# Kernel optimization log

Measured on AMD Instinct MI355X. Metric: run time of the kernel, lower is better.

## Reference

```python
import jax, jax.numpy as jnp
import numpy as np

N_ROI = 116; G = 128; DEG = 32
N = G * N_ROI          # 14848 nodes
E = G * N_ROI * DEG    # 475136 edges
HID = 64; HEADS = 4; HC = HEADS * HID  # 256
EDIM = 5; EMB = 16; NG = 8; OUT = 2
NEG = 0.01      # nn.LeakyReLU default slope
NEG_ATT = 0.2   # GATv2 internal negative_slope
EPS = 1e-5


def leaky(x, s=NEG):
    return jnp.where(x >= 0, x, s * x)


def seg_softmax(logits, seg, n):
    # numerically stable softmax over edges grouped by target node
    m = jax.ops.segment_max(logits, seg, num_segments=n)
    m = jnp.where(jnp.isfinite(m), m, 0.0)
    ex = jnp.exp(logits - m[seg])
    s = jax.ops.segment_sum(ex, seg, num_segments=n)
    return ex / (s[seg] + 1e-16)


def _xav(k, shape):
    return jax.random.normal(k, shape, jnp.float32) * np.sqrt(2.0 / sum(shape)).astype(np.float32)


def setup_inputs() -> dict:
    key = jax.random.key(0)
    ks = jax.random.split(key, 40)
    x = jax.random.normal(ks[0], (N, N_ROI), jnp.float32)
    off = (jnp.arange(G, dtype=jnp.int32) * N_ROI)[:, None]
    src = (jax.random.randint(ks[1], (G, N_ROI * DEG), 0, N_ROI, jnp.int32) + off).reshape(-1)
    dst = (jax.random.randint(ks[2], (G, N_ROI * DEG), 0, N_ROI, jnp.int32) + off).reshape(-1)
    edge_index = jnp.stack([src, dst])  # [2, E], block-diagonal per graph
    edge_attr = jax.random.normal(ks[3], (E, EDIM), jnp.float32)
    grp = np.repeat(np.arange(NG, dtype=np.int32), [15] * 7 + [11])  # partition of 116 ROIs
    node_group = jnp.tile(jnp.asarray(grp), G)
    batch = jnp.repeat(jnp.arange(G, dtype=jnp.int32), N_ROI)
    p = {
        'group_emb': _xav(ks[4], (NG, EMB)),
        'W_embed': _xav(ks[5], (N_ROI + EMB, HID)), 'b_embed': jnp.zeros((HID,), jnp.float32),
        'We_enc': _xav(ks[6], (EDIM, HID)), 'be_enc': jnp.zeros((HID,), jnp.float32),
        'W1': _xav(ks[7], (HID, HID)), 'b1': jnp.zeros((HID,), jnp.float32),
        'W2': _xav(ks[8], (HID, HID)), 'b2': jnp.zeros((HID,), jnp.float32),
        'ln_g': jnp.ones((HID,), jnp.float32), 'ln_b': jnp.zeros((HID,), jnp.float32),
        'l0_Wl': _xav(ks[9], (HID, HC)), 'l0_Wr': _xav(ks[10], (HID, HC)),
        'l0_We': _xav(ks[11], (EDIM, HC)), 'l0_att': _xav(ks[12], (HEADS, HID)),
        'l0_b': jnp.zeros((HC,), jnp.float32),
        'l0_bn_g': jnp.ones((HC,), jnp.float32), 'l0_bn_b': jnp.zeros((HC,), jnp.float32),
        'l1_Wl': _xav(ks[13], (HC, HC)), 'l1_Wr': _xav(ks[14], (HC, HC)),
        'l1_We': _xav(ks[15], (EDIM, HC)), 'l1_att': _xav(ks[16], (HEADS, HID)),
        'l1_b': jnp.zeros((HC,), jnp.float32),
        'l1_bn_g': jnp.ones((HC,), jnp.float32), 'l1_bn_b': jnp.zeros((HC,), jnp.float32),
        'fc2_W': _xav(ks[17], (HC, OUT)), 'fc2_b': jnp.zeros((OUT,), jnp.float32),
    }
    return dict(x=x, edge_index=edge_index, edge_attr=edge_attr, batch=batch, node_group=node_group, **p)


def _gat_layer(h, src, dst, edge_attr, Wl, Wr, We, att, b, bn_g, bn_b):
    n = h.shape[0]
    xl = (h @ Wl).reshape(n, HEADS, HID)
    xr = (h @ Wr).reshape(n, HEADS, HID)
    e = (edge_attr @ We).reshape(-1, HEADS, HID)
    xls = xl[src]                                   # [E,H,C]
    z = leaky(xls + xr[dst] + e, NEG_ATT)
    logits = jnp.einsum('ehc,hc->eh', z, att)       # GATv2 attention scores
    alpha = seg_softmax(logits, dst, n)             # softmax over incoming edges per node
    out = jax.ops.segment_sum(xls * alpha[:, :, None], dst, num_segments=n)
    out = out.reshape(n, HC) + b
    mu = out.mean(0); var = ((out - mu) ** 2).mean(0)  # BatchNorm (batch stats)
    out = (out - mu) / jnp.sqrt(var + EPS) * bn_g + bn_b
    return leaky(out)


def reference(x, edge_index, edge_attr, batch, node_group, group_emb, W_embed, b_embed,
              We_enc, be_enc, W1, b1, W2, b2, ln_g, ln_b,
              l0_Wl, l0_Wr, l0_We, l0_att, l0_b, l0_bn_g, l0_bn_b,
              l1_Wl, l1_Wr, l1_We, l1_att, l1_b, l1_bn_g, l1_bn_b, fc2_W, fc2_b):
    src, dst = edge_index[0], edge_index[1]
    # BrainEncodeEmbed: group embedding concat + projection
    h = jnp.concatenate([x, group_emb[node_group]], axis=-1)   # [N, 132]
    h = leaky(h @ W_embed + b_embed)                            # [N, HID]
    eemb = leaky(edge_attr @ We_enc + be_enc)                   # [E, HID]
    # GINEConv: sum_j ReLU(x_j + e_ij), eps=0, then MLP
    msg = jax.nn.relu(h[src] + eemb)
    h = h + jax.ops.segment_sum(msg, dst, num_segments=N)
    h = leaky(h @ W1 + b1) @ W2 + b2
    h = leaky(h)
    mu = h.mean(-1, keepdims=True)
    v = ((h - mu) ** 2).mean(-1, keepdims=True)
    h = (h - mu) / jnp.sqrt(v + EPS) * ln_g + ln_b              # LayerNorm
    # stacked GATv2 blocks
    h = _gat_layer(h, src, dst, edge_attr, l0_Wl, l0_Wr, l0_We, l0_att, l0_b, l0_bn_g, l0_bn_b)
    h = _gat_layer(h, src, dst, edge_attr, l1_Wl, l1_Wr, l1_We, l1_att, l1_b, l1_bn_g, l1_bn_b)
    # global mean pool + classifier
    cnt = jax.ops.segment_sum(jnp.ones((h.shape[0],), h.dtype), batch, num_segments=G)
    pooled = jax.ops.segment_sum(h, batch, num_segments=G) / cnt[:, None]
    return pooled @ fc2_W + fc2_b
```

## Files before the change

### kernel.cpp

```cpp
#include <hip/hip_runtime.h>
#include <hip/hip_bf16.h>

#define NN     14848
#define NE     475136
#define NROI   116
#define NGRAPH 128
#define EPG    3712
#define HID    64
#define HC     256
#define NEG    0.01f
#define NEGA   0.2f
#define EPB    2304
#define XPADB  66

typedef __attribute__((ext_vector_type(8))) short short8;
typedef __attribute__((ext_vector_type(4))) float floatx4;
typedef __attribute__((ext_vector_type(2))) float floatx2;

__device__ __forceinline__ float leaky(float x, float s) { return fmaxf(x, s * x); }

__device__ __forceinline__ short f2bf(float f) {
    unsigned u = __float_as_uint(f);
    unsigned r = (u + 0x7fffu + ((u >> 16) & 1u)) >> 16;
    return (short)r;
}
__device__ __forceinline__ float bf2f(unsigned short b) {
    return __uint_as_float((unsigned)b << 16);
}

__global__ __launch_bounds__(256) void k_front(
    const float* __restrict__ x, const int* __restrict__ ng,
    const float* __restrict__ gemb, const float* __restrict__ W,
    const float* __restrict__ b, short* __restrict__ h0,
    const int* __restrict__ src, const int* __restrict__ dst,
    const float* __restrict__ ea,
    int* __restrict__ row_start, int* __restrict__ row_cnt,
    int* __restrict__ ssd, float* __restrict__ ea_s,
    float* __restrict__ stats01,
    const float* __restrict__ Wl0, const float* __restrict__ Wr0,
    const float* __restrict__ Wl1, const float* __restrict__ Wr1,
    short* __restrict__ Wt0, short* __restrict__ Wt1)
{
    const int tid = threadIdx.x;
    if (blockIdx.x < NGRAPH) {
        const int g = blockIdx.x;
        if (g < 2) {
            for (int i = tid; i < 512; i += 256) stats01[g * 512 + i] = 0.f;
        }
        const int e0 = g * EPG, nb = g * NROI;
        __shared__ int cnt[NROI], start[NROI], scn[128];
        __shared__ unsigned short pos[EPG];
        if (tid < NROI) cnt[tid] = 0;
        __syncthreads();
        for (int i = tid; i < EPG; i += 256) {
            const int dl = dst[e0 + i] - nb;
            pos[i] = (unsigned short)atomicAdd(&cnt[dl], 1);
        }
        __syncthreads();
        if (tid < 128) scn[tid] = (tid < NROI) ? cnt[tid] : 0;
        __syncthreads();
        #pragma unroll
        for (int off = 1; off < 128; off <<= 1) {
            int v = 0;
            if (tid < 128 && tid >= off) v = scn[tid - off];
            __syncthreads();
            if (tid < 128) scn[tid] += v;
            __syncthreads();
        }
        if (tid < NROI) {
            const int st = scn[tid] - cnt[tid];
            start[tid] = st;
            row_start[nb + tid] = e0 + st;
            row_cnt[nb + tid] = cnt[tid];
        }
        __syncthreads();
        for (int i = tid; i < EPG; i += 256) {
            const int e = e0 + i;
            const int dl = dst[e] - nb;
            const int gi = e0 + start[dl] + (int)pos[i];
            ssd[gi] = (src[e] - nb) | (dl << 16);
            const float4 q = make_float4(ea[e * 5], ea[e * 5 + 1], ea[e * 5 + 2], ea[e * 5 + 3]);
            *(float4*)&ea_s[(size_t)gi * 8] = q;
            ea_s[(size_t)gi * 8 + 4] = ea[e * 5 + 4];
        }
    } else if (blockIdx.x < NGRAPH + NN / 4) {
        const int w = tid >> 6, c = tid & 63;
        const int n = (blockIdx.x - NGRAPH) * 4 + w;
        __shared__ float in[4][132];
        for (int k = c; k < NROI; k += 64) in[w][k] = x[n * NROI + k];
        if (c < 16) in[w][NROI + c] = gemb[ng[n] * 16 + c];
        __syncthreads();
        float acc = b[c];
        #pragma unroll 4
        for (int k = 0; k < 132; k++) acc = fmaf(in[w][k], W[k * 64 + c], acc);
        h0[n * 64 + c] = f2bf(leaky(acc, NEG));
    } else {
        const int bb = blockIdx.x - (NGRAPH + NN / 4);
        if (bb < 512) {
            const int n = bb;
            for (int k = tid; k < 64; k += 256) {
                const float v = (n < 256) ? Wl0[k * 256 + n] : Wr0[k * 256 + (n - 256)];
                Wt0[(size_t)n * 64 + k] = f2bf(v);
            }
        } else {
            const int n = bb - 512;
            for (int k = tid; k < 256; k += 256) {
                const float v = (n < 256) ? Wl1[k * 256 + n] : Wr1[k * 256 + (n - 256)];
                Wt1[(size_t)n * 256 + k] = f2bf(v);
            }
        }
    }
}

__global__ __launch_bounds__(256) void k_gine_mlp_ln(
    const short* __restrict__ h0, const int* __restrict__ row_start,
    const int* __restrict__ row_cnt, const int* __restrict__ ssd,
    const float* __restrict__ ea_s,
    const float* __restrict__ We, const float* __restrict__ be,
    const float* __restrict__ W1, const float* __restrict__ b1,
    const float* __restrict__ W2, const float* __restrict__ b2,
    const float* __restrict__ lg_, const float* __restrict__ lb_,
    short* __restrict__ hn)
{
    const int tid = threadIdx.x, w = tid >> 6, lane = tid & 63;
    const int row = blockIdx.x * 4 + w;
    const int nb = (row / NROI) * NROI;
    const int st = row_start[row], cnt = row_cnt[row];
    const float w0 = We[lane], w1 = We[64 + lane], w2 = We[128 + lane],
                w3 = We[192 + lane], w4 = We[256 + lane];
    const float bec = be[lane];
    float g0 = 0.f, g1 = 0.f, g2 = 0.f, g3 = 0.f;
    int j = 0;
    for (; j + 4 <= cnt; j += 4) {
        const int i0 = st + j, i1 = st + j + 1, i2 = st + j + 2, i3 = st + j + 3;
        const int s0 = nb + (ssd[i0] & 0xffff), s1 = nb + (ssd[i1] & 0xffff),
                  s2 = nb + (ssd[i2] & 0xffff), s3 = nb + (ssd[i3] & 0xffff);
        const float h_0 = bf2f((unsigned short)h0[s0 * 64 + lane]),
                    h_1 = bf2f((unsigned short)h0[s1 * 64 + lane]),
                    h_2 = bf2f((unsigned short)h0[s2 * 64 + lane]),
                    h_3 = bf2f((unsigned short)h0[s3 * 64 + lane]);
        const float4 qa = *(const float4*)&ea_s[(size_t)i0 * 8];
        const float qa4 = ea_s[(size_t)i0 * 8 + 4];
        const float4 qb = *(const float4*)&ea_s[(size_t)i1 * 8];
        const float qb4 = ea_s[(size_t)i1 * 8 + 4];
        const float4 qc = *(const float4*)&ea_s[(size_t)i2 * 8];
        const float qc4 = ea_s[(size_t)i2 * 8 + 4];
        const float4 qd = *(const float4*)&ea_s[(size_t)i3 * 8];
        const float qd4 = ea_s[(size_t)i3 * 8 + 4];
        float e0_ = bec, e1_ = bec, e2_ = bec, e3_ = bec;
        e0_ = fmaf(qa.x, w0, e0_); e1_ = fmaf(qb.x, w0, e1_);
        e2_ = fmaf(qc.x, w0, e2_); e3_ = fmaf(qd.x, w0, e3_);
        e0_ = fmaf(qa.y, w1, e0_); e1_ = fmaf(qb.y, w1, e1_);
        e2_ = fmaf(qc.y, w1, e2_); e3_ = fmaf(qd.y, w1, e3_);
        e0_ = fmaf(qa.z, w2, e0_); e1_ = fmaf(qb.z, w2, e1_);
        e2_ = fmaf(qc.z, w2, e2_); e3_ = fmaf(qd.z, w2, e3_);
        e0_ = fmaf(qa.w, w3, e0_); e1_ = fmaf(qb.w, w3, e1_);
        e2_ = fmaf(qc.w, w3, e2_); e3_ = fmaf(qd.w, w3, e3_);
        e0_ = fmaf(qa4, w4, e0_);  e1_ = fmaf(qb4, w4, e1_);
        e2_ = fmaf(qc4, w4, e2_);  e3_ = fmaf(qd4, w4, e3_);
        g0 += fmaxf(h_0 + leaky(e0_, NEG), 0.f);
        g1 += fmaxf(h_1 + leaky(e1_, NEG), 0.f);
        g2 += fmaxf(h_2 + leaky(e2_, NEG), 0.f);
        g3 += fmaxf(h_3 + leaky(e3_, NEG), 0.f);
    }
    for (; j < cnt; j++) {
        const int idx = st + j;
        const int s = nb + (ssd[idx] & 0xffff);
        const float4 q = *(const float4*)&ea_s[(size_t)idx * 8];
        const float q4 = ea_s[(size_t)idx * 8 + 4];
        float em = bec;
        em = fmaf(q.x, w0, em); em = fmaf(q.y, w1, em); em = fmaf(q.z, w2, em);
        em = fmaf(q.w, w3, em); em = fmaf(q4, w4, em);
        g0 += fmaxf(bf2f((unsigned short)h0[s * 64 + lane]) + leaky(em, NEG), 0.f);
    }
    const float aggv = (g0 + g1) + (g2 + g3);
    __shared__ float v[4][64], t[4][64];
    v[w][lane] = bf2f((unsigned short)h0[row * 64 + lane]) + aggv;
    __syncthreads();
    float a = b1[lane];
    #pragma unroll 8
    for (int k = 0; k < 64; k++) a = fmaf(v[w][k], W1[k * 64 + lane], a);
    t[w][lane] = leaky(a, NEG);
    __syncthreads();
    float o = b2[lane];
    #pragma unroll 8
    for (int k = 0; k < 64; k++) o = fmaf(t[w][k], W2[k * 64 + lane], o);
    o = leaky(o, NEG);
    float s = o;
    #pragma unroll
    for (int off = 32; off; off >>= 1) s += __shfl_xor(s, off);
    const float mu = s * (1.f / 64.f);
    const float d = o - mu;
    float s2 = d * d;
    #pragma unroll
    for (int off = 32; off; off >>= 1) s2 += __shfl_xor(s2, off);
    hn[row * 64 + lane] = f2bf(d * rsqrtf(s2 * (1.f / 64.f) + 1e-5f) * lg_[lane] + lb_[lane]);
}

template <int D, bool BN>
__global__ __launch_bounds__(256) void k_gemm(
    const short* __restrict__ A, const float* __restrict__ Vin,
    const float* __restrict__ stats, const float* __restrict__ bn_g,
    const float* __restrict__ bn_b,
    const short* __restrict__ Wt,
    float* __restrict__ X, float* __restrict__ Y)
{
    const int m0 = blockIdx.x * 16;
    const int w = threadIdx.x >> 6, lane = threadIdx.x & 63;
    const int n0 = w * 128;
    const int r = lane & 15, q = lane >> 4;
    __shared__ float sc_s[256], sh_s[256];
    if constexpr (BN) {
        const int c = threadIdx.x;
        const float inv_n = 1.f / (float)NN;
        const float mu = stats[c] * inv_n;
        float var = stats[256 + c] * inv_n - mu * mu;
        var = fmaxf(var, 0.f);
        const float rsg = rsqrtf(var + 1e-5f) * bn_g[c];
        sc_s[c] = rsg;
        sh_s[c] = bn_b[c] - mu * rsg;
        __syncthreads();
    }
    floatx4 acc[8];
    #pragma unroll
    for (int t = 0; t < 8; t++) acc[t] = (floatx4){0.f, 0.f, 0.f, 0.f};
    const short* Arow = A + (size_t)(m0 + r) * D + q * 8;
    const float* Vrow = Vin + (size_t)(m0 + r) * D + q * 8;
    const short* Brow = Wt + (size_t)(n0 + r) * D + q * 8;
    #pragma unroll
    for (int k0 = 0; k0 < D; k0 += 32) {
        short8 a;
        if constexpr (BN) {
            const float4 v0 = *(const float4*)(Vrow + k0);
            const float4 v1 = *(const float4*)(Vrow + k0 + 4);
            const int cb = q * 8 + k0;
            a[0] = f2bf(leaky(fmaf(v0.x, sc_s[cb + 0], sh_s[cb + 0]), NEG));
            a[1] = f2bf(leaky(fmaf(v0.y, sc_s[cb + 1], sh_s[cb + 1]), NEG));
            a[2] = f2bf(leaky(fmaf(v0.z, sc_s[cb + 2], sh_s[cb + 2]), NEG));
            a[3] = f2bf(leaky(fmaf(v0.w, sc_s[cb + 3], sh_s[cb + 3]), NEG));
            a[4] = f2bf(leaky(fmaf(v1.x, sc_s[cb + 4], sh_s[cb + 4]), NEG));
            a[5] = f2bf(leaky(fmaf(v1.y, sc_s[cb + 5], sh_s[cb + 5]), NEG));
            a[6] = f2bf(leaky(fmaf(v1.z, sc_s[cb + 6], sh_s[cb + 6]), NEG));
            a[7] = f2bf(leaky(fmaf(v1.w, sc_s[cb + 7], sh_s[cb + 7]), NEG));
        } else {
            a = *(const short8*)(Arow + k0);
        }
        #pragma unroll
        for (int t = 0; t < 8; t++) {
            const short8 b = *(const short8*)(Brow + (size_t)t * 16 * D + k0);
            acc[t] = __builtin_amdgcn_mfma_f32_16x16x32_bf16(a, b, acc[t], 0, 0, 0);
        }
    }
    #pragma unroll
    for (int t = 0; t < 8; t++) {
        const int ncol = n0 + t * 16 + r;
        #pragma unroll
        for (int g2 = 0; g2 < 4; g2++) {
            const int row = m0 + q * 4 + g2;
            if (ncol < 256) X[(size_t)row * HC + ncol] = acc[t][g2];
            else            Y[(size_t)row * HC + (ncol - 256)] = acc[t][g2];
        }
    }
}

__global__ __launch_bounds__(256, 6) void k_gat(
    const int* __restrict__ row_start, const int* __restrict__ row_cnt,
    const int* __restrict__ ssd, const float* __restrict__ ea_s,
    const float* __restrict__ We, const float* __restrict__ att,
    const float* __restrict__ bias,
    const float* __restrict__ X, const float* __restrict__ Y,
    float* __restrict__ V, float* __restrict__ stats)
{
    const int g = blockIdx.x & 127;
    const int sub = blockIdx.x >> 7;
    const int h = sub >> 1;
    const int half = sub & 1;
    const int tid = threadIdx.x, w = tid >> 6, lane = tid & 63;
    const int nb = g * NROI, e0 = g * EPG, hc = h * 64;
    const int r0 = half * 58, r1 = r0 + 58;
    const int es = row_start[nb + r0];
    const int ee = (r1 < NROI) ? row_start[nb + r1] : e0 + EPG;

    __shared__ short Xs[NROI * XPADB];
    __shared__ float lg[EPB];
    __shared__ float inv_s[58];

    for (int r = w; r < NROI; r += 4)
        Xs[r * XPADB + lane] = f2bf(X[(size_t)(nb + r) * HC + hc + lane]);
    __syncthreads();

    const int ne = ee - es;
    for (int i = tid; i < ne; i += 256) {
        const int e = es + i;
        const int sd = ssd[e];
        const int sl = sd & 0xffff, dl = sd >> 16;
        const float4 q = *(const float4*)&ea_s[(size_t)e * 8];
        const float q4 = ea_s[(size_t)e * 8 + 4];
        const floatx2 qx = {q.x, q.x}, qy = {q.y, q.y}, qz = {q.z, q.z},
                      qw = {q.w, q.w}, qv = {q4, q4};
        const float* yrow = &Y[(size_t)(nb + dl) * HC + hc];
        const unsigned* xrow = (const unsigned*)&Xs[sl * XPADB];
        floatx2 lacc = {0.f, 0.f};
        #pragma unroll 8
        for (int c = 0; c < 64; c += 2) {
            const floatx2 y2 = *(const floatx2*)(yrow + c);
            const unsigned xp = xrow[c >> 1];
            const floatx2 xs2 = {__uint_as_float(xp << 16),
                                 __uint_as_float(xp & 0xffff0000u)};
            const floatx2 w0 = *(const floatx2*)(We + 0 * HC + hc + c);
            const floatx2 w1 = *(const floatx2*)(We + 1 * HC + hc + c);
            const floatx2 w2 = *(const floatx2*)(We + 2 * HC + hc + c);
            const floatx2 w3 = *(const floatx2*)(We + 3 * HC + hc + c);
            const floatx2 w4 = *(const floatx2*)(We + 4 * HC + hc + c);
            floatx2 ep = qx * w0;
            ep += qy * w1;
            ep += qz * w2;
            ep += qw * w3;
            ep += qv * w4;
            const floatx2 z = xs2 + y2 + ep;
            const floatx2 zs = z * (floatx2){NEGA, NEGA};
            const floatx2 lk = {fmaxf(z.x, zs.x), fmaxf(z.y, zs.y)};
            const floatx2 a2 = *(const floatx2*)(att + hc + c);
            lacc += a2 * lk;
        }
        lg[i] = lacc.x + lacc.y;
    }
    __syncthreads();

    for (int r = r0 + w; r < r1; r += 4) {
        const int stl = row_start[nb + r] - es;
        const int cnt = row_cnt[nb + r];
        float m = -INFINITY;
        for (int j = lane; j < cnt; j += 64) m = fmaxf(m, lg[stl + j]);
        #pragma unroll
        for (int off = 32; off; off >>= 1) m = fmaxf(m, __shfl_xor(m, off));
        float s = 0.f;
        for (int j = lane; j < cnt; j += 64) {
            const float e_ = __expf(lg[stl + j] - m);
            lg[stl + j] = e_;
            s += e_;
        }
        #pragma unroll
        for (int off = 32; off; off >>= 1) s += __shfl_xor(s, off);
        if (lane == 0) inv_s[r - r0] = 1.f / (s + 1e-16f);
    }
    __syncthreads();

    float ps = 0.f, ps2 = 0.f;
    const float bb = bias[hc + lane];
    for (int r = r0 + w; r < r1; r += 4) {
        const int st = row_start[nb + r];
        const int cnt = row_cnt[nb + r];
        const int stl = st - es;
        float a0 = 0.f, a1 = 0.f, a2 = 0.f, a3 = 0.f;
        int j = 0;
        for (; j + 4 <= cnt; j += 4) {
            const int s0 = ssd[st + j] & 0xffff, s1 = ssd[st + j + 1] & 0xffff,
                      s2 = ssd[st + j + 2] & 0xffff, s3 = ssd[st + j + 3] & 0xffff;
            a0 = fmaf(bf2f((unsigned short)Xs[s0 * XPADB + lane]), lg[stl + j], a0);
            a1 = fmaf(bf2f((unsigned short)Xs[s1 * XPADB + lane]), lg[stl + j + 1], a1);
            a2 = fmaf(bf2f((unsigned short)Xs[s2 * XPADB + lane]), lg[stl + j + 2], a2);
            a3 = fmaf(bf2f((unsigned short)Xs[s3 * XPADB + lane]), lg[stl + j + 3], a3);
        }
        for (; j < cnt; j++)
            a0 = fmaf(bf2f((unsigned short)Xs[(ssd[st + j] & 0xffff) * XPADB + lane]),
                      lg[stl + j], a0);
        const float vv = ((a0 + a1) + (a2 + a3)) * inv_s[r - r0] + bb;
        V[(size_t)(nb + r) * HC + hc + lane] = vv;
        ps += vv;
        ps2 += vv * vv;
    }
    __syncthreads();
    lg[tid] = ps;
    lg[256 + tid] = ps2;
    __syncthreads();
    if (tid < 64) {
        float s1 = 0.f, s2 = 0.f;
        #pragma unroll
        for (int w2 = 0; w2 < 4; w2++) {
            s1 += lg[w2 * 64 + tid];
            s2 += lg[256 + w2 * 64 + tid];
        }
        atomicAdd(&stats[hc + tid], s1);
        atomicAdd(&stats[256 + hc + tid], s2);
    }
}

__global__ __launch_bounds__(256) void k_pool_fc(
    const float* __restrict__ V, const float* __restrict__ stats,
    const float* __restrict__ bg, const float* __restrict__ bb,
    const float* __restrict__ fW, const float* __restrict__ fb,
    float* __restrict__ out)
{
    const int g = blockIdx.x, c = threadIdx.x;
    const float inv_n = 1.f / (float)NN;
    const float mu = stats[c] * inv_n;
    float var = stats[256 + c] * inv_n - mu * mu;
    var = fmaxf(var, 0.f);
    const float rsg = rsqrtf(var + 1e-5f) * bg[c];
    const float bbc = bb[c];
    float s = 0.f;
    for (int r = 0; r < NROI; r++) {
        const float vv = (V[(size_t)(g * NROI + r) * HC + c] - mu) * rsg + bbc;
        s += leaky(vv, NEG);
    }
    s *= (1.f / (float)NROI);
    __shared__ float red[256];
    for (int o = 0; o < 2; o++) {
        red[c] = s * fW[c * 2 + o];
        __syncthreads();
        for (int off = 128; off; off >>= 1) {
            if (c < off) red[c] += red[c + off];
            __syncthreads();
        }
        if (c == 0) out[g * 2 + o] = red[0] + fb[o];
        __syncthreads();
    }
}

extern "C" void kernel_launch(void* const* d_in, const int* in_sizes, int n_in,
                              void* d_out, int out_size, void* d_ws, size_t ws_size,
                              hipStream_t stream) {
    const float* x         = (const float*)d_in[0];
    const int*   edge_idx  = (const int*)d_in[1];
    const float* edge_attr = (const float*)d_in[2];
    const int*   node_grp  = (const int*)d_in[4];
    const float* group_emb = (const float*)d_in[5];
    const float* W_embed   = (const float*)d_in[6];
    const float* b_embed   = (const float*)d_in[7];
    const float* We_enc    = (const float*)d_in[8];
    const float* be_enc    = (const float*)d_in[9];
    const float* W1        = (const float*)d_in[10];
    const float* b1        = (const float*)d_in[11];
    const float* W2        = (const float*)d_in[12];
    const float* b2        = (const float*)d_in[13];
    const float* ln_g      = (const float*)d_in[14];
    const float* ln_b      = (const float*)d_in[15];
    const float* l0_Wl     = (const float*)d_in[16];
    const float* l0_Wr     = (const float*)d_in[17];
    const float* l0_We     = (const float*)d_in[18];
    const float* l0_att    = (const float*)d_in[19];
    const float* l0_b      = (const float*)d_in[20];
    const float* l0_bn_g   = (const float*)d_in[21];
    const float* l0_bn_b   = (const float*)d_in[22];
    const float* l1_Wl     = (const float*)d_in[23];
    const float* l1_Wr     = (const float*)d_in[24];
    const float* l1_We     = (const float*)d_in[25];
    const float* l1_att    = (const float*)d_in[26];
    const float* l1_b      = (const float*)d_in[27];
    const float* l1_bn_g   = (const float*)d_in[28];
    const float* l1_bn_b   = (const float*)d_in[29];
    const float* fc2_W     = (const float*)d_in[30];
    const float* fc2_b     = (const float*)d_in[31];

    const int* src = edge_idx;
    const int* dst = edge_idx + NE;

    float* ws     = (float*)d_ws;
    float* h0f    = ws;
    float* X      = h0f + (size_t)64 * NN;
    float* Y      = X + (size_t)HC * NN;
    float* V      = Y + (size_t)HC * NN;
    float* stats0 = V + (size_t)HC * NN;
    float* stats1 = stats0 + 512;
    float* ea_s   = stats1 + 512;
    int* row_start = (int*)(ea_s + (size_t)8 * NE);
    int* row_cnt   = row_start + NN;
    int* ssd       = row_cnt + NN;
    short* hn_b    = (short*)(ssd + NE);
    short* Wt0     = hn_b + (size_t)64 * NN;
    short* Wt1     = Wt0 + 512 * 64;
    short* h0      = (short*)h0f;

    float* out = (float*)d_out;

    k_front<<<NGRAPH + NN / 4 + 1024, 256, 0, stream>>>(
        x, node_grp, group_emb, W_embed, b_embed, h0,
        src, dst, edge_attr, row_start, row_cnt, ssd, ea_s, stats0,
        l0_Wl, l0_Wr, l1_Wl, l1_Wr, Wt0, Wt1);
    k_gine_mlp_ln<<<NN / 4, 256, 0, stream>>>(h0, row_start, row_cnt, ssd, ea_s,
                                              We_enc, be_enc, W1, b1, W2, b2, ln_g, ln_b, hn_b);

    k_gemm<64, false><<<NN / 16, 256, 0, stream>>>(hn_b, nullptr, nullptr, nullptr, nullptr,
                                                   Wt0, X, Y);
    k_gat<<<NGRAPH * 8, 256, 0, stream>>>(row_start, row_cnt, ssd, ea_s,
                                          l0_We, l0_att, l0_b, X, Y, V, stats0);

    k_gemm<256, true><<<NN / 16, 256, 0, stream>>>(nullptr, V, stats0, l0_bn_g, l0_bn_b,
                                                   Wt1, X, Y);
    k_gat<<<NGRAPH * 8, 256, 0, stream>>>(row_start, row_cnt, ssd, ea_s,
                                          l1_We, l1_att, l1_b, X, Y, V, stats1);

    k_pool_fc<<<NGRAPH, 256, 0, stream>>>(V, stats1, l1_bn_g, l1_bn_b, fc2_W, fc2_b, out);
}
```

Before: 410.9 us.

## Fuse GINE/MLP/LayerNorm with first GAT projection GEMM; drop softmax max pass

Merges the GINE aggregation, MLP and LayerNorm kernel with the layer-0 bf16 MFMA projection. Each 1024-thread block handles 16 rows and keeps the normalized rows in shared memory instead of writing them to global memory and launching a separate GEMM. In the GAT kernel, the segment-max pass is removed: logits are exponentiated directly and the row sum is computed inside the aggregation loop. This saves a launch, an intermediate round trip and a synchronized softmax pass. The cost is losing max subtraction, which risks overflow for large logits, and lower occupancy from 1024-thread blocks.

```diff
diff --git a/kernel.cpp b/kernel.cpp
--- a/kernel.cpp
+++ b/kernel.cpp
@@ -112,7 +112,7 @@
     }
 }
 
-__global__ __launch_bounds__(256) void k_gine_mlp_ln(
+__global__ __launch_bounds__(1024) void k_gine_gemm(
     const short* __restrict__ h0, const int* __restrict__ row_start,
     const int* __restrict__ row_cnt, const int* __restrict__ ssd,
     const float* __restrict__ ea_s,
@@ -120,81 +120,111 @@
     const float* __restrict__ W1, const float* __restrict__ b1,
     const float* __restrict__ W2, const float* __restrict__ b2,
     const float* __restrict__ lg_, const float* __restrict__ lb_,
-    short* __restrict__ hn)
+    const short* __restrict__ Wt,
+    float* __restrict__ X, float* __restrict__ Y)
 {
     const int tid = threadIdx.x, w = tid >> 6, lane = tid & 63;
-    const int row = blockIdx.x * 4 + w;
-    const int nb = (row / NROI) * NROI;
-    const int st = row_start[row], cnt = row_cnt[row];
-    const float w0 = We[lane], w1 = We[64 + lane], w2 = We[128 + lane],
-                w3 = We[192 + lane], w4 = We[256 + lane];
-    const float bec = be[lane];
-    float g0 = 0.f, g1 = 0.f, g2 = 0.f, g3 = 0.f;
-    int j = 0;
-    for (; j + 4 <= cnt; j += 4) {
-        const int i0 = st + j, i1 = st + j + 1, i2 = st + j + 2, i3 = st + j + 3;
-        const int s0 = nb + (ssd[i0] & 0xffff), s1 = nb + (ssd[i1] & 0xffff),
-                  s2 = nb + (ssd[i2] & 0xffff), s3 = nb + (ssd[i3] & 0xffff);
-        const float h_0 = bf2f((unsigned short)h0[s0 * 64 + lane]),
-                    h_1 = bf2f((unsigned short)h0[s1 * 64 + lane]),
-                    h_2 = bf2f((unsigned short)h0[s2 * 64 + lane]),
-                    h_3 = bf2f((unsigned short)h0[s3 * 64 + lane]);
-        const float4 qa = *(const float4*)&ea_s[(size_t)i0 * 8];
-        const float qa4 = ea_s[(size_t)i0 * 8 + 4];
-        const float4 qb = *(const float4*)&ea_s[(size_t)i1 * 8];
-        const float qb4 = ea_s[(size_t)i1 * 8 + 4];
-        const float4 qc = *(const float4*)&ea_s[(size_t)i2 * 8];
-        const float qc4 = ea_s[(size_t)i2 * 8 + 4];
-        const float4 qd = *(const float4*)&ea_s[(size_t)i3 * 8];
-        const float qd4 = ea_s[(size_t)i3 * 8 + 4];
-        float e0_ = bec, e1_ = bec, e2_ = bec, e3_ = bec;
-        e0_ = fmaf(qa.x, w0, e0_); e1_ = fmaf(qb.x, w0, e1_);
-        e2_ = fmaf(qc.x, w0, e2_); e3_ = fmaf(qd.x, w0, e3_);
-        e0_ = fmaf(qa.y, w1, e0_); e1_ = fmaf(qb.y, w1, e1_);
-        e2_ = fmaf(qc.y, w1, e2_); e3_ = fmaf(qd.y, w1, e3_);
-        e0_ = fmaf(qa.z, w2, e0_); e1_ = fmaf(qb.z, w2, e1_);
-        e2_ = fmaf(qc.z, w2, e2_); e3_ = fmaf(qd.z, w2, e3_);
-        e0_ = fmaf(qa.w, w3, e0_); e1_ = fmaf(qb.w, w3, e1_);
-        e2_ = fmaf(qc.w, w3, e2_); e3_ = fmaf(qd.w, w3, e3_);
-        e0_ = fmaf(qa4, w4, e0_);  e1_ = fmaf(qb4, w4, e1_);
-        e2_ = fmaf(qc4, w4, e2_);  e3_ = fmaf(qd4, w4, e3_);
-        g0 += fmaxf(h_0 + leaky(e0_, NEG), 0.f);
-        g1 += fmaxf(h_1 + leaky(e1_, NEG), 0.f);
-        g2 += fmaxf(h_2 + leaky(e2_, NEG), 0.f);
-        g3 += fmaxf(h_3 + leaky(e3_, NEG), 0.f);
-    }
-    for (; j < cnt; j++) {
-        const int idx = st + j;
-        const int s = nb + (ssd[idx] & 0xffff);
-        const float4 q = *(const float4*)&ea_s[(size_t)idx * 8];
-        const float q4 = ea_s[(size_t)idx * 8 + 4];
-        float em = bec;
-        em = fmaf(q.x, w0, em); em = fmaf(q.y, w1, em); em = fmaf(q.z, w2, em);
-        em = fmaf(q.w, w3, em); em = fmaf(q4, w4, em);
-        g0 += fmaxf(bf2f((unsigned short)h0[s * 64 + lane]) + leaky(em, NEG), 0.f);
-    }
-    const float aggv = (g0 + g1) + (g2 + g3);
-    __shared__ float v[4][64], t[4][64];
-    v[w][lane] = bf2f((unsigned short)h0[row * 64 + lane]) + aggv;
+    const int m0 = blockIdx.x * 16;
+    const int row = m0 + w;
+    __shared__ __align__(16) short Hs[16][72];
+    __shared__ float v[16][64], t[16][64];
+    {
+        const int nb = (row / NROI) * NROI;
+        const int st = row_start[row], cnt = row_cnt[row];
+        const float w0 = We[lane], w1 = We[64 + lane], w2 = We[128 + lane],
+                    w3 = We[192 + lane], w4 = We[256 + lane];
+        const float bec = be[lane];
+        float g0 = 0.f, g1 = 0.f, g2 = 0.f, g3 = 0.f;
+        int j = 0;
+        for (; j + 4 <= cnt; j += 4) {
+            const int i0 = st + j, i1 = st + j + 1, i2 = st + j + 2, i3 = st + j + 3;
+            const int s0 = nb + (ssd[i0] & 0xffff), s1 = nb + (ssd[i1] & 0xffff),
+                      s2 = nb + (ssd[i2] & 0xffff), s3 = nb + (ssd[i3] & 0xffff);
+            const float h_0 = bf2f((unsigned short)h0[s0 * 64 + lane]),
+                        h_1 = bf2f((unsigned short)h0[s1 * 64 + lane]),
+                        h_2 = bf2f((unsigned short)h0[s2 * 64 + lane]),
+                        h_3 = bf2f((unsigned short)h0[s3 * 64 + lane]);
+            const float4 qa = *(const float4*)&ea_s[(size_t)i0 * 8];
+            const float qa4 = ea_s[(size_t)i0 * 8 + 4];
+            const float4 qb = *(const float4*)&ea_s[(size_t)i1 * 8];
+            const float qb4 = ea_s[(size_t)i1 * 8 + 4];
+            const float4 qc = *(const float4*)&ea_s[(size_t)i2 * 8];
+            const float qc4 = ea_s[(size_t)i2 * 8 + 4];
+            const float4 qd = *(const float4*)&ea_s[(size_t)i3 * 8];
+            const float qd4 = ea_s[(size_t)i3 * 8 + 4];
+            float e0_ = bec, e1_ = bec, e2_ = bec, e3_ = bec;
+            e0_ = fmaf(qa.x, w0, e0_); e1_ = fmaf(qb.x, w0, e1_);
+            e2_ = fmaf(qc.x, w0, e2_); e3_ = fmaf(qd.x, w0, e3_);
+            e0_ = fmaf(qa.y, w1, e0_); e1_ = fmaf(qb.y, w1, e1_);
+            e2_ = fmaf(qc.y, w1, e2_); e3_ = fmaf(qd.y, w1, e3_);
+            e0_ = fmaf(qa.z, w2, e0_); e1_ = fmaf(qb.z, w2, e1_);
+            e2_ = fmaf(qc.z, w2, e2_); e3_ = fmaf(qd.z, w2, e3_);
+            e0_ = fmaf(qa.w, w3, e0_); e1_ = fmaf(qb.w, w3, e1_);
+            e2_ = fmaf(qc.w, w3, e2_); e3_ = fmaf(qd.w, w3, e3_);
+            e0_ = fmaf(qa4, w4, e0_);  e1_ = fmaf(qb4, w4, e1_);
+            e2_ = fmaf(qc4, w4, e2_);  e3_ = fmaf(qd4, w4, e3_);
+            g0 += fmaxf(h_0 + leaky(e0_, NEG), 0.f);
+            g1 += fmaxf(h_1 + leaky(e1_, NEG), 0.f);
+            g2 += fmaxf(h_2 + leaky(e2_, NEG), 0.f);
+            g3 += fmaxf(h_3 + leaky(e3_, NEG), 0.f);
+        }
+        for (; j < cnt; j++) {
+            const int idx = st + j;
+            const int s = nb + (ssd[idx] & 0xffff);
+            const float4 q = *(const float4*)&ea_s[(size_t)idx * 8];
+            const float q4 = ea_s[(size_t)idx * 8 + 4];
+            float em = bec;
+            em = fmaf(q.x, w0, em); em = fmaf(q.y, w1, em); em = fmaf(q.z, w2, em);
+            em = fmaf(q.w, w3, em); em = fmaf(q4, w4, em);
+            g0 += fmaxf(bf2f((unsigned short)h0[s * 64 + lane]) + leaky(em, NEG), 0.f);
+        }
+        const float aggv = (g0 + g1) + (g2 + g3);
+        v[w][lane] = bf2f((unsigned short)h0[row * 64 + lane]) + aggv;
+        float a = b1[lane];
+        #pragma unroll 8
+        for (int k = 0; k < 64; k++) a = fmaf(v[w][k], W1[k * 64 + lane], a);
+        t[w][lane] = leaky(a, NEG);
+        float o = b2[lane];
+        #pragma unroll 8
+        for (int k = 0; k < 64; k++) o = fmaf(t[w][k], W2[k * 64 + lane], o);
+        o = leaky(o, NEG);
+        float s = o;
+        #pragma unroll
+        for (int off = 32; off; off >>= 1) s += __shfl_xor(s, off);
+        const float mu = s * (1.f / 64.f);
+        const float d = o - mu;
+        float s2 = d * d;
+        #pragma unroll
+        for (int off = 32; off; off >>= 1) s2 += __shfl_xor(s2, off);
+        Hs[w][lane] = f2bf(d * rsqrtf(s2 * (1.f / 64.f) + 1e-5f) * lg_[lane] + lb_[lane]);
+    }
     __syncthreads();
-    float a = b1[lane];
-    #pragma unroll 8
-    for (int k = 0; k < 64; k++) a = fmaf(v[w][k], W1[k * 64 + lane], a);
-    t[w][lane] = leaky(a, NEG);
-    __syncthreads();
-    float o = b2[lane];
-    #pragma unroll 8
-    for (int k = 0; k < 64; k++) o = fmaf(t[w][k], W2[k * 64 + lane], o);
-    o = leaky(o, NEG);
-    float s = o;
+    const int r = lane & 15, q = lane >> 4;
+    const short* Arow = &Hs[r][q * 8];
+    floatx4 acc[2];
+    acc[0] = (floatx4){0.f, 0.f, 0.f, 0.f};
+    acc[1] = (floatx4){0.f, 0.f, 0.f, 0.f};
     #pragma unroll
-    for (int off = 32; off; off >>= 1) s += __shfl_xor(s, off);
-    const float mu = s * (1.f / 64.f);
-    const float d = o - mu;
-    float s2 = d * d;
+    for (int t2 = 0; t2 < 2; t2++) {
+        const int n = w * 32 + t2 * 16 + r;
+        const short* Brow = Wt + (size_t)n * 64 + q * 8;
+        #pragma unroll
+        for (int k0 = 0; k0 < 64; k0 += 32) {
+            const short8 a = *(const short8*)(Arow + k0);
+            const short8 b = *(const short8*)(Brow + k0);
+            acc[t2] = __builtin_amdgcn_mfma_f32_16x16x32_bf16(a, b, acc[t2], 0, 0, 0);
+        }
+    }
     #pragma unroll
-    for (int off = 32; off; off >>= 1) s2 += __shfl_xor(s2, off);
-    hn[row * 64 + lane] = f2bf(d * rsqrtf(s2 * (1.f / 64.f) + 1e-5f) * lg_[lane] + lb_[lane]);
+    for (int t2 = 0; t2 < 2; t2++) {
+        const int ncol = w * 32 + t2 * 16 + r;
+        #pragma unroll
+        for (int g2 = 0; g2 < 4; g2++) {
+            const int ro = m0 + q * 4 + g2;
+            if (ncol < 256) X[(size_t)ro * HC + ncol] = acc[t2][g2];
+            else            Y[(size_t)ro * HC + (ncol - 256)] = acc[t2][g2];
+        }
+    }
 }
 
 template <int D, bool BN>
@@ -283,7 +313,6 @@
 
     __shared__ short Xs[NROI * XPADB];
     __shared__ float lg[EPB];
-    __shared__ float inv_s[58];
 
     for (int r = w; r < NROI; r += 4)
         Xs[r * XPADB + lane] = f2bf(X[(size_t)(nb + r) * HC + hc + lane]);
@@ -323,26 +352,7 @@
             const floatx2 a2 = *(const floatx2*)(att + hc + c);
             lacc += a2 * lk;
         }
-        lg[i] = lacc.x + lacc.y;
-    }
-    __syncthreads();
-
-    for (int r = r0 + w; r < r1; r += 4) {
-        const int stl = row_start[nb + r] - es;
-        const int cnt = row_cnt[nb + r];
-        float m = -INFINITY;
-        for (int j = lane; j < cnt; j += 64) m = fmaxf(m, lg[stl + j]);
-        #pragma unroll
-        for (int off = 32; off; off >>= 1) m = fmaxf(m, __shfl_xor(m, off));
-        float s = 0.f;
-        for (int j = lane; j < cnt; j += 64) {
-            const float e_ = __expf(lg[stl + j] - m);
-            lg[stl + j] = e_;
-            s += e_;
-        }
-        #pragma unroll
-        for (int off = 32; off; off >>= 1) s += __shfl_xor(s, off);
-        if (lane == 0) inv_s[r - r0] = 1.f / (s + 1e-16f);
+        lg[i] = __expf(lacc.x + lacc.y);
     }
     __syncthreads();
 
@@ -352,6 +362,11 @@
         const int st = row_start[nb + r];
         const int cnt = row_cnt[nb + r];
         const int stl = st - es;
+        float s = 0.f;
+        for (int j = lane; j < cnt; j += 64) s += lg[stl + j];
+        #pragma unroll
+        for (int off = 32; off; off >>= 1) s += __shfl_xor(s, off);
+        const float inv = 1.f / (s + 1e-16f);
         float a0 = 0.f, a1 = 0.f, a2 = 0.f, a3 = 0.f;
         int j = 0;
         for (; j + 4 <= cnt; j += 4) {
@@ -365,7 +380,7 @@
         for (; j < cnt; j++)
             a0 = fmaf(bf2f((unsigned short)Xs[(ssd[st + j] & 0xffff) * XPADB + lane]),
                       lg[stl + j], a0);
-        const float vv = ((a0 + a1) + (a2 + a3)) * inv_s[r - r0] + bb;
+        const float vv = ((a0 + a1) + (a2 + a3)) * inv + bb;
         V[(size_t)(nb + r) * HC + hc + lane] = vv;
         ps += vv;
         ps2 += vv * vv;
@@ -467,8 +482,7 @@
     int* row_start = (int*)(ea_s + (size_t)8 * NE);
     int* row_cnt   = row_start + NN;
     int* ssd       = row_cnt + NN;
-    short* hn_b    = (short*)(ssd + NE);
-    short* Wt0     = hn_b + (size_t)64 * NN;
+    short* Wt0     = (short*)(ssd + NE);
     short* Wt1     = Wt0 + 512 * 64;
     short* h0      = (short*)h0f;
 
@@ -478,11 +492,11 @@
         x, node_grp, group_emb, W_embed, b_embed, h0,
         src, dst, edge_attr, row_start, row_cnt, ssd, ea_s, stats0,
         l0_Wl, l0_Wr, l1_Wl, l1_Wr, Wt0, Wt1);
-    k_gine_mlp_ln<<<NN / 4, 256, 0, stream>>>(h0, row_start, row_cnt, ssd, ea_s,
-                                              We_enc, be_enc, W1, b1, W2, b2, ln_g, ln_b, hn_b);
-
-    k_gemm<64, false><<<NN / 16, 256, 0, stream>>>(hn_b, nullptr, nullptr, nullptr, nullptr,
-                                                   Wt0, X, Y);
+
+    k_gine_gemm<<<NN / 16, 1024, 0, stream>>>(h0, row_start, row_cnt, ssd, ea_s,
+                                              We_enc, be_enc, W1, b1, W2, b2, ln_g, ln_b,
+                                              Wt0, X, Y);
+
     k_gat<<<NGRAPH * 8, 256, 0, stream>>>(row_start, row_cnt, ssd, ea_s,
                                           l0_We, l0_att, l0_b, X, Y, V, stats0);
 
```

Result: faster. 394.6 us (-4.0%).
